# Performance work log

Hardware: AMD Instinct MI355X
Metric: run time of the kernel (lower is better)

The kernel has to match this reference:

```python
import jax, jax.numpy as jnp
import numpy as np
from jax.ops import segment_sum

N = 100000   # nodes
E = 6400000  # edges
D = 128      # input/output feature dim (d)
H = 15       # hidden width hard-coded in the module


def setup_inputs() -> dict:
    key = jax.random.key(0)
    ks = jax.random.split(key, 10)
    x = jax.random.normal(ks[0], (N, D), dtype=jnp.float32)
    edge_index = jax.random.randint(ks[1], (2, E), 0, N, dtype=jnp.int64)
    def glorot(k, shape):
        lim = np.sqrt(6.0 / (shape[0] + shape[1]))
        return jax.random.uniform(k, shape, jnp.float32, -lim, lim)
    W1 = glorot(ks[2], (D, H)); b1 = jnp.zeros((H,), jnp.float32)
    W2 = glorot(ks[3], (H, H)); b2 = jnp.zeros((H,), jnp.float32)
    W3 = glorot(ks[4], (H, H)); b3 = jnp.zeros((H,), jnp.float32)
    Wc = glorot(ks[5], (H, D)); bc = jnp.zeros((D,), jnp.float32)
    return {"x": x, "edge_index": edge_index,
            "W1": W1, "b1": b1, "W2": W2, "b2": b2,
            "W3": W3, "b3": b3, "Wc": Wc, "bc": bc}


def _gcn_norm(edge_index, n_nodes):
    # PyG GCNConv default: add self-loops, symmetric normalization.
    loops = jnp.arange(n_nodes, dtype=edge_index.dtype)
    row = jnp.concatenate([edge_index[0], loops])  # source
    col = jnp.concatenate([edge_index[1], loops])  # target (aggregation index)
    deg = segment_sum(jnp.ones_like(col, dtype=jnp.float32), col, num_segments=n_nodes)
    dinv = jnp.where(deg > 0, jax.lax.rsqrt(deg), 0.0)
    norm = dinv[row] * dinv[col]  # [E+N]
    return row, col, norm


def _gcn_conv(x, W, b, row, col, norm, n_nodes):
    h = x @ W                                   # [N, out]
    msg = h[row] * norm[:, None]                # gather + scale
    agg = segment_sum(msg, col, num_segments=n_nodes)
    return agg + b


def reference(x, edge_index, W1, b1, W2, b2, W3, b3, Wc, bc):
    row, col, norm = _gcn_norm(edge_index, N)
    h = jax.nn.relu(_gcn_conv(x, W1, b1, row, col, norm, N))
    h = jax.nn.relu(_gcn_conv(h, W2, b2, row, col, norm, N))
    h = jax.nn.relu(_gcn_conv(h, W3, b3, row, col, norm, N))
    return h @ Wc + bc
```

## Files before the change

### kernel.cpp

```cpp
#include <hip/hip_runtime.h>
#include <hip/hip_fp16.h>

#define DD 128
#define HH 15
#define BSHIFT 8
#define BUCK (1 << BSHIFT)
#define NBUCK 391
#define CAP 18432
#define CHUNK 4096
#define ABLK 512


__global__ __launch_bounds__(512) void init_gcur(int* __restrict__ gcur) {
    int i = threadIdx.x;
    if (i < NBUCK) gcur[i] = i * CAP;
}


__global__ __launch_bounds__(512) void partA(const int* __restrict__ row, const int* __restrict__ col,
                      int* __restrict__ gcur, unsigned* __restrict__ tmp, int E) {
    __shared__ int histo[NBUCK];
    __shared__ int hbase[NBUCK];
    __shared__ int hscan[NBUCK];
    __shared__ int wsum[8];
    __shared__ int s_total;
    __shared__ unsigned staged[CHUNK];
    __shared__ int saddr[CHUNK];
    int tid = threadIdx.x;
    int start = blockIdx.x * CHUNK;
    for (int i = tid; i < NBUCK; i += ABLK) histo[i] = 0;
    __syncthreads();
    unsigned pk[8]; unsigned short lp[8]; unsigned short bk[8];
    for (int k = 0; k < 8; ++k) {
        int e = start + k * ABLK + tid;
        bk[k] = 0xFFFF;
        if (e < E) {
            int cc = col[e];
            int b = cc >> BSHIFT;
            int rr = row[e];
            pk[k] = (unsigned)rr | ((unsigned)(cc & (BUCK - 1)) << 17);
            bk[k] = (unsigned short)b;
            lp[k] = (unsigned short)atomicAdd(&histo[b], 1);
        }
    }
    __syncthreads();
    int lane = tid & 63, wv = tid >> 6;
    int v = (tid < NBUCK) ? histo[tid] : 0;
    int s = v;
#pragma unroll
    for (int off = 1; off < 64; off <<= 1) {
        int u = __shfl_up(s, off, 64);
        if (lane >= off) s += u;
    }
    if (lane == 63) wsum[wv] = s;
    __syncthreads();
    if (tid == 0) {
        int r = 0;
        for (int i = 0; i < 8; ++i) { int u = wsum[i]; wsum[i] = r; r += u; }
        s_total = r;
    }
    __syncthreads();
    if (tid < NBUCK) {
        int excl = s + wsum[wv] - v;
        hscan[tid] = excl;
        if (v > 0) hbase[tid] = atomicAdd(&gcur[tid], v);
    }
    __syncthreads();
    for (int k = 0; k < 8; ++k) {
        if (bk[k] != 0xFFFF) {
            int b = bk[k];
            int slot = hscan[b] + lp[k];
            saddr[slot]  = min(hbase[b] + lp[k], NBUCK * CAP - 1);
            staged[slot] = pk[k];
        }
    }
    __syncthreads();
    int tot = s_total;
    for (int k = tid; k < tot; k += ABLK)
        tmp[saddr[k]] = staged[k];
}


__global__ __launch_bounds__(512) void scanC(const int* __restrict__ gcur,
                                             int* __restrict__ cbase,
                                             int* __restrict__ rowptr, int N) {
    __shared__ int wsum[8];
    int t = threadIdx.x, lane = t & 63, wv = t >> 6;
    int v = 0;
    if (t < NBUCK) v = min(gcur[t] - t * CAP, CAP);
    int s = v;
#pragma unroll
    for (int off = 1; off < 64; off <<= 1) {
        int u = __shfl_up(s, off, 64);
        if (lane >= off) s += u;
    }
    if (lane == 63) wsum[wv] = s;
    __syncthreads();
    int total = 0;
    if (t == 0) { int r = 0; for (int i = 0; i < 8; ++i) { int u = wsum[i]; wsum[i] = r; r += u; } total = r; }
    __syncthreads();
    if (t < NBUCK) cbase[t] = s + wsum[wv] - v;
    if (t == 0) { cbase[NBUCK] = total; rowptr[N] = total; }
}


__global__ __launch_bounds__(1024) void partB(const int* __restrict__ cbase, const unsigned* __restrict__ tmp,
                      int* __restrict__ rowptr, float* __restrict__ dinv,
                      int* __restrict__ csr_row, int N) {
    __shared__ int hist[BUCK];
    __shared__ int cur[BUCK];
    __shared__ int wsum[4];
    int b = blockIdx.x;
    int node0 = b << BSHIFT;
    int nn = min(BUCK, N - node0);
    int tid = threadIdx.x;
    if (tid < BUCK) hist[tid] = 0;
    __syncthreads();
    int base = cbase[b];
    int cnt  = cbase[b + 1] - base;
    const unsigned* te = tmp + (size_t)b * CAP;
    for (int e = tid; e < cnt; e += 1024)
        atomicAdd(&hist[te[e] >> 17], 1);
    __syncthreads();
    int lane = tid & 63, wv = tid >> 6;
    int d0 = (tid < BUCK) ? hist[tid] : 0;
    int s = d0;
#pragma unroll
    for (int off = 1; off < 64; off <<= 1) {
        int u = __shfl_up(s, off, 64);
        if (lane >= off) s += u;
    }
    if (tid < BUCK && lane == 63) wsum[wv] = s;
    __syncthreads();
    if (tid == 0) { int r = 0; for (int i = 0; i < 4; ++i) { int u = wsum[i]; wsum[i] = r; r += u; } }
    __syncthreads();
    if (tid < BUCK) {
        int excl = s + wsum[wv] - d0;
        cur[tid] = base + excl;
        if (tid < nn) {
            rowptr[node0 + tid] = base + excl;
            dinv[node0 + tid] = rsqrtf((float)(d0 + 1));
        }
    }
    __syncthreads();
    for (int e = tid; e < cnt; e += 1024) {
        unsigned v2 = te[e];
        int lc = (int)(v2 >> 17);
        int pos = atomicAdd(&cur[lc], 1);
        csr_row[pos] = (int)(v2 & 0x1FFFFu);
    }
}


__global__ void gemm1_kernel(const float* __restrict__ x, const float* __restrict__ W,
                             const float* __restrict__ dinv, __half* __restrict__ hs) {
    __shared__ float Wl[DD * HH];
    __shared__ float xs[16 * DD];
    int tid = threadIdx.x;
    for (int i = tid; i < DD * HH; i += 256) Wl[i] = W[i];
    size_t base = (size_t)blockIdx.x * 16 * DD;
    const float4* xv = (const float4*)(x + base);
    float4* xsv = (float4*)xs;
    xsv[tid]       = xv[tid];
    xsv[tid + 256] = xv[tid + 256];
    __syncthreads();
    int g = tid >> 4, f = tid & 15;
    int n = blockIdx.x * 16 + g;
    float val = 0.f;
    if (f < HH) {
        const float* xrow = xs + g * DD;
        float acc = 0.f;
#pragma unroll 8
        for (int k = 0; k < DD; ++k) acc += xrow[k] * Wl[k * HH + f];
        val = acc * dinv[n];
    }
    hs[(size_t)n * 16 + f] = __float2half(val);
}


__global__ void gemm_mid_kernel(const float* __restrict__ agg, const float* __restrict__ bias,
                                const float* __restrict__ W, const float* __restrict__ dinv,
                                __half* __restrict__ hs) {
    __shared__ float Wl[HH * HH];
    __shared__ float s_in[256];
    int tid = threadIdx.x;
    if (tid < HH * HH) Wl[tid] = W[tid];
    int n0 = blockIdx.x * 16;
    int g = tid >> 4, f = tid & 15;
    int n = n0 + g;
    if (f < HH) {
        float v = agg[(size_t)n * 16 + f] + bias[f];
        s_in[tid] = v > 0.f ? v : 0.f;
    }
    __syncthreads();
    float val = 0.f;
    if (f < HH) {
        const float* in = s_in + g * 16;
        float acc = 0.f;
#pragma unroll
        for (int k = 0; k < HH; ++k) acc += in[k] * Wl[k * HH + f];
        val = acc * dinv[n];
    }
    hs[(size_t)n * 16 + f] = __float2half(val);
}


struct alignas(16) H8 { __half2 h[4]; };

__device__ inline void acc8(float4& a0, float4& a1, const H8& v) {
    float2 f0 = __half22float2(v.h[0]);
    float2 f1 = __half22float2(v.h[1]);
    float2 f2 = __half22float2(v.h[2]);
    float2 f3 = __half22float2(v.h[3]);
    a0.x += f0.x; a0.y += f0.y; a0.z += f1.x; a0.w += f1.y;
    a1.x += f2.x; a1.y += f2.y; a1.z += f3.x; a1.w += f3.y;
}

__device__ inline float4 shfl_down4(float4 v, int off) {
    v.x = __shfl_down(v.x, off, 64);
    v.y = __shfl_down(v.y, off, 64);
    v.z = __shfl_down(v.z, off, 64);
    v.w = __shfl_down(v.w, off, 64);
    return v;
}

__global__ void aggregate_kernel(const int* __restrict__ rowptr, const int* __restrict__ csr_row,
                                 const float* __restrict__ dinv, const __half* __restrict__ hs,
                                 float* __restrict__ agg, int N) {
    int wid = (blockIdx.x * 256 + threadIdx.x) >> 6;
    int lane = threadIdx.x & 63;
    int sub = lane & 15;
    int c = wid * 4 + (lane >> 4);
    int q = sub & 1, eg = sub >> 1;
    int s = 0, epe = 0;
    if (c < N) { s = rowptr[c]; epe = rowptr[c + 1]; }
    const H8* h8 = (const H8*)hs;
    float4 a0 = make_float4(0.f, 0.f, 0.f, 0.f), a1 = a0;
    int e = s + eg;
    for (; e + 24 < epe; e += 32) {
        int i0 = csr_row[e];
        int i1 = csr_row[e + 8];
        int i2 = csr_row[e + 16];
        int i3 = csr_row[e + 24];
        H8 v0 = h8[((size_t)i0 << 1) + q];
        H8 v1 = h8[((size_t)i1 << 1) + q];
        H8 v2 = h8[((size_t)i2 << 1) + q];
        H8 v3 = h8[((size_t)i3 << 1) + q];
        acc8(a0, a1, v0); acc8(a0, a1, v1); acc8(a0, a1, v2); acc8(a0, a1, v3);
    }
    for (; e < epe; e += 8) {
        H8 v = h8[((size_t)csr_row[e] << 1) + q];
        acc8(a0, a1, v);
    }
#define RED4(off) { float4 t0_ = shfl_down4(a0, off); float4 t1_ = shfl_down4(a1, off); \
                    a0.x += t0_.x; a0.y += t0_.y; a0.z += t0_.z; a0.w += t0_.w; \
                    a1.x += t1_.x; a1.y += t1_.y; a1.z += t1_.z; a1.w += t1_.w; }
    RED4(8) RED4(4) RED4(2)
#undef RED4
    if (sub < 2 && c < N) {
        float d = dinv[c];
        H8 sv = h8[((size_t)c << 1) + q];
        float2 s0 = __half22float2(sv.h[0]);
        float2 s1 = __half22float2(sv.h[1]);
        float2 s2 = __half22float2(sv.h[2]);
        float2 s3 = __half22float2(sv.h[3]);
        float4 o0, o1;
        o0.x = d * (a0.x + s0.x); o0.y = d * (a0.y + s0.y);
        o0.z = d * (a0.z + s1.x); o0.w = d * (a0.w + s1.y);
        o1.x = d * (a1.x + s2.x); o1.y = d * (a1.y + s2.y);
        o1.z = d * (a1.z + s3.x); o1.w = d * (a1.w + s3.y);
        ((float4*)agg)[((size_t)c << 2) + q * 2]     = o0;
        ((float4*)agg)[((size_t)c << 2) + q * 2 + 1] = o1;
    }
}


__global__ void gemm_out_kernel(const float* __restrict__ agg, const float* __restrict__ bias,
                                const float* __restrict__ Wc, const float* __restrict__ bc,
                                float* __restrict__ out, int N) {
    __shared__ float Wl[HH * DD];
    __shared__ float s_in[256];
    int tid = threadIdx.x;
    for (int i = tid; i < HH * DD; i += 256) Wl[i] = Wc[i];
    int n0 = blockIdx.x * 16;
    {
        int gg = tid >> 4, ff = tid & 15;
        int n = n0 + gg;
        float v = 0.f;
        if (ff < HH && n < N) v = agg[(size_t)n * 16 + ff] + bias[ff];
        s_in[tid] = v > 0.f ? v : 0.f;
    }
    __syncthreads();
    int g = tid >> 7, f = tid & 127;
    float bcf = bc[f];
#pragma unroll
    for (int it = 0; it < 8; ++it) {
        int nl = it * 2 + g;
        int n = n0 + nl;
        const float* in = s_in + nl * 16;
        float acc = bcf;
#pragma unroll
        for (int k = 0; k < HH; ++k) acc += in[k] * Wl[k * DD + f];
        if (n < N) out[(size_t)n * DD + f] = acc;
    }
}


extern "C" void kernel_launch(void* const* d_in, const int* in_sizes, int n_in,
                              void* d_out, int out_size, void* d_ws, size_t ws_size,
                              hipStream_t stream) {
    const float* x  = (const float*)d_in[0];
    const int*   ei = (const int*)d_in[1];
    const float* W1 = (const float*)d_in[2];
    const float* b1 = (const float*)d_in[3];
    const float* W2 = (const float*)d_in[4];
    const float* b2 = (const float*)d_in[5];
    const float* W3 = (const float*)d_in[6];
    const float* b3 = (const float*)d_in[7];
    const float* Wc = (const float*)d_in[8];
    const float* bc = (const float*)d_in[9];
    float* out = (float*)d_out;

    int N = in_sizes[0] / DD;
    int E = in_sizes[1] / 2;
    const int* row = ei;
    const int* col = ei + E;

    char* ws = (char*)d_ws;
    size_t off = 0;
    auto alloc = [&](size_t bytes) {
        void* p = ws + off;
        off += (bytes + 255) & ~(size_t)255;
        return p;
    };
    float*    dinv    = (float*)   alloc((size_t)N * 4);
    int*      rowptr  = (int*)     alloc((size_t)(N + 1) * 4);
    int*      gcur    = (int*)     alloc((size_t)NBUCK * 4);
    int*      cbase   = (int*)     alloc((size_t)(NBUCK + 1) * 4);
    int*      csr_row = (int*)     alloc((size_t)E * 4 + 256);
    unsigned* tmp     = (unsigned*)alloc((size_t)NBUCK * CAP * 4);
    (void)n_in; (void)out_size; (void)ws_size;

    __half* hs  = (__half*)tmp;
    float*  agg = (float*)((char*)tmp + (size_t)N * 32);

    int eblocks = (E + CHUNK - 1) / CHUNK;

    init_gcur<<<1, 512, 0, stream>>>(gcur);
    partA<<<eblocks, ABLK, 0, stream>>>(row, col, gcur, tmp, E);
    scanC<<<1, 512, 0, stream>>>(gcur, cbase, rowptr, N);
    partB<<<NBUCK, 1024, 0, stream>>>(cbase, tmp, rowptr, dinv, csr_row, N);

    int nb16 = (N + 15) / 16;
    int aggblocks = (N + 15) / 16;

    gemm1_kernel<<<nb16, 256, 0, stream>>>(x, W1, dinv, hs);
    aggregate_kernel<<<aggblocks, 256, 0, stream>>>(rowptr, csr_row, dinv, hs, agg, N);
    gemm_mid_kernel<<<nb16, 256, 0, stream>>>(agg, b1, W2, dinv, hs);
    aggregate_kernel<<<aggblocks, 256, 0, stream>>>(rowptr, csr_row, dinv, hs, agg, N);
    gemm_mid_kernel<<<nb16, 256, 0, stream>>>(agg, b2, W3, dinv, hs);
    aggregate_kernel<<<aggblocks, 256, 0, stream>>>(rowptr, csr_row, dinv, hs, agg, N);
    gemm_out_kernel<<<nb16, 256, 0, stream>>>(agg, b3, Wc, bc, out, N);
}
```

Before: 398.9 us.

## Fuse bias, ReLU and hidden GEMM into aggregation kernel epilogue

Folds the mid-layer bias+ReLU+15x15 matmul into the aggregation kernel's epilogue, using wave shuffles to broadcast each node's 16 aggregated features. This removes two gemm_mid launches and the fp32 agg round trip between them. It also ping-pongs between two fp16 feature buffers and deepens the gather unroll from 4 to 8 loads in flight. The cost is more registers (launch bounds of 2 blocks per CU) and extra shuffles per node.

```diff
diff --git a/kernel.cpp b/kernel.cpp
--- a/kernel.cpp
+++ b/kernel.cpp
@@ -178,40 +178,11 @@
 }
 
 
-__global__ void gemm_mid_kernel(const float* __restrict__ agg, const float* __restrict__ bias,
-                                const float* __restrict__ W, const float* __restrict__ dinv,
-                                __half* __restrict__ hs) {
-    __shared__ float Wl[HH * HH];
-    __shared__ float s_in[256];
-    int tid = threadIdx.x;
-    if (tid < HH * HH) Wl[tid] = W[tid];
-    int n0 = blockIdx.x * 16;
-    int g = tid >> 4, f = tid & 15;
-    int n = n0 + g;
-    if (f < HH) {
-        float v = agg[(size_t)n * 16 + f] + bias[f];
-        s_in[tid] = v > 0.f ? v : 0.f;
-    }
-    __syncthreads();
-    float val = 0.f;
-    if (f < HH) {
-        const float* in = s_in + g * 16;
-        float acc = 0.f;
-#pragma unroll
-        for (int k = 0; k < HH; ++k) acc += in[k] * Wl[k * HH + f];
-        val = acc * dinv[n];
-    }
-    hs[(size_t)n * 16 + f] = __float2half(val);
-}
-
-
-struct alignas(16) H8 { __half2 h[4]; };
-
-__device__ inline void acc8(float4& a0, float4& a1, const H8& v) {
-    float2 f0 = __half22float2(v.h[0]);
-    float2 f1 = __half22float2(v.h[1]);
-    float2 f2 = __half22float2(v.h[2]);
-    float2 f3 = __half22float2(v.h[3]);
+__device__ inline void accU(float4& a0, float4& a1, const uint4& u) {
+    float2 f0 = __half22float2(*(const __half2*)&u.x);
+    float2 f1 = __half22float2(*(const __half2*)&u.y);
+    float2 f2 = __half22float2(*(const __half2*)&u.z);
+    float2 f3 = __half22float2(*(const __half2*)&u.w);
     a0.x += f0.x; a0.y += f0.y; a0.z += f1.x; a0.w += f1.y;
     a1.x += f2.x; a1.y += f2.y; a1.z += f3.x; a1.w += f3.y;
 }
@@ -224,54 +195,110 @@
     return v;
 }
 
-__global__ void aggregate_kernel(const int* __restrict__ rowptr, const int* __restrict__ csr_row,
-                                 const float* __restrict__ dinv, const __half* __restrict__ hs,
-                                 float* __restrict__ agg, int N) {
-    int wid = (blockIdx.x * 256 + threadIdx.x) >> 6;
-    int lane = threadIdx.x & 63;
+template <int FUSE>
+__global__ __launch_bounds__(256, 2)
+void aggregate_kernel(const int* __restrict__ rowptr, const int* __restrict__ csr_row,
+                      const float* __restrict__ dinv, const __half* __restrict__ hs,
+                      float* __restrict__ aggout,
+                      const float* __restrict__ bias, const float* __restrict__ W,
+                      __half* __restrict__ hsout, int N) {
+    __shared__ float Wl[16 * 16];
+    __shared__ float bs[16];
+    int tid = threadIdx.x;
+    if (FUSE) {
+        {
+            int k = tid >> 4, f = tid & 15;
+            Wl[tid] = (k < HH && f < HH) ? W[k * HH + f] : 0.f;
+        }
+        if (tid < 16) bs[tid] = (tid < HH) ? bias[tid] : 0.f;
+        __syncthreads();
+    }
+    int wid = (blockIdx.x * 256 + tid) >> 6;
+    int lane = tid & 63;
     int sub = lane & 15;
     int c = wid * 4 + (lane >> 4);
     int q = sub & 1, eg = sub >> 1;
     int s = 0, epe = 0;
     if (c < N) { s = rowptr[c]; epe = rowptr[c + 1]; }
-    const H8* h8 = (const H8*)hs;
+    const uint4* h8 = (const uint4*)hs;
     float4 a0 = make_float4(0.f, 0.f, 0.f, 0.f), a1 = a0;
     int e = s + eg;
-    for (; e + 24 < epe; e += 32) {
-        int i0 = csr_row[e];
-        int i1 = csr_row[e + 8];
-        int i2 = csr_row[e + 16];
-        int i3 = csr_row[e + 24];
-        H8 v0 = h8[((size_t)i0 << 1) + q];
-        H8 v1 = h8[((size_t)i1 << 1) + q];
-        H8 v2 = h8[((size_t)i2 << 1) + q];
-        H8 v3 = h8[((size_t)i3 << 1) + q];
-        acc8(a0, a1, v0); acc8(a0, a1, v1); acc8(a0, a1, v2); acc8(a0, a1, v3);
-    }
-    for (; e < epe; e += 8) {
-        H8 v = h8[((size_t)csr_row[e] << 1) + q];
-        acc8(a0, a1, v);
+    for (; e + 56 < epe; e += 64) {
+        int i0 = csr_row[e];      int i1 = csr_row[e + 8];
+        int i2 = csr_row[e + 16]; int i3 = csr_row[e + 24];
+        int i4 = csr_row[e + 32]; int i5 = csr_row[e + 40];
+        int i6 = csr_row[e + 48]; int i7 = csr_row[e + 56];
+        uint4 v0 = h8[((size_t)i0 << 1) + q];
+        uint4 v1 = h8[((size_t)i1 << 1) + q];
+        uint4 v2 = h8[((size_t)i2 << 1) + q];
+        uint4 v3 = h8[((size_t)i3 << 1) + q];
+        uint4 v4 = h8[((size_t)i4 << 1) + q];
+        uint4 v5 = h8[((size_t)i5 << 1) + q];
+        uint4 v6 = h8[((size_t)i6 << 1) + q];
+        uint4 v7 = h8[((size_t)i7 << 1) + q];
+        accU(a0, a1, v0); accU(a0, a1, v1); accU(a0, a1, v2); accU(a0, a1, v3);
+        accU(a0, a1, v4); accU(a0, a1, v5); accU(a0, a1, v6); accU(a0, a1, v7);
+    }
+    for (; e + 8 < epe; e += 16) {
+        int i0 = csr_row[e]; int i1 = csr_row[e + 8];
+        uint4 v0 = h8[((size_t)i0 << 1) + q];
+        uint4 v1 = h8[((size_t)i1 << 1) + q];
+        accU(a0, a1, v0); accU(a0, a1, v1);
+    }
+    if (e < epe) {
+        uint4 v0 = h8[((size_t)csr_row[e] << 1) + q];
+        accU(a0, a1, v0);
     }
 #define RED4(off) { float4 t0_ = shfl_down4(a0, off); float4 t1_ = shfl_down4(a1, off); \
                     a0.x += t0_.x; a0.y += t0_.y; a0.z += t0_.z; a0.w += t0_.w; \
                     a1.x += t1_.x; a1.y += t1_.y; a1.z += t1_.z; a1.w += t1_.w; }
     RED4(8) RED4(4) RED4(2)
 #undef RED4
+    float d = (c < N) ? dinv[c] : 0.f;
+    float4 o0 = make_float4(0.f, 0.f, 0.f, 0.f), o1 = o0;
     if (sub < 2 && c < N) {
-        float d = dinv[c];
-        H8 sv = h8[((size_t)c << 1) + q];
-        float2 s0 = __half22float2(sv.h[0]);
-        float2 s1 = __half22float2(sv.h[1]);
-        float2 s2 = __half22float2(sv.h[2]);
-        float2 s3 = __half22float2(sv.h[3]);
-        float4 o0, o1;
+        uint4 su = h8[((size_t)c << 1) + q];
+        float2 s0 = __half22float2(*(const __half2*)&su.x);
+        float2 s1 = __half22float2(*(const __half2*)&su.y);
+        float2 s2 = __half22float2(*(const __half2*)&su.z);
+        float2 s3 = __half22float2(*(const __half2*)&su.w);
         o0.x = d * (a0.x + s0.x); o0.y = d * (a0.y + s0.y);
         o0.z = d * (a0.z + s1.x); o0.w = d * (a0.w + s1.y);
         o1.x = d * (a1.x + s2.x); o1.y = d * (a1.y + s2.y);
         o1.z = d * (a1.z + s3.x); o1.w = d * (a1.w + s3.y);
-        ((float4*)agg)[((size_t)c << 2) + q * 2]     = o0;
-        ((float4*)agg)[((size_t)c << 2) + q * 2 + 1] = o1;
-    }
+    }
+    if (!FUSE) {
+        if (sub < 2 && c < N) {
+            ((float4*)aggout)[((size_t)c << 2) + q * 2]     = o0;
+            ((float4*)aggout)[((size_t)c << 2) + q * 2 + 1] = o1;
+        }
+        return;
+    }
+    if (sub < 2) {
+        int bb = q * 8;
+        o0.x += bs[bb + 0]; o0.y += bs[bb + 1]; o0.z += bs[bb + 2]; o0.w += bs[bb + 3];
+        o1.x += bs[bb + 4]; o1.y += bs[bb + 5]; o1.z += bs[bb + 6]; o1.w += bs[bb + 7];
+        o0.x = fmaxf(o0.x, 0.f); o0.y = fmaxf(o0.y, 0.f);
+        o0.z = fmaxf(o0.z, 0.f); o0.w = fmaxf(o0.w, 0.f);
+        o1.x = fmaxf(o1.x, 0.f); o1.y = fmaxf(o1.y, 0.f);
+        o1.z = fmaxf(o1.z, 0.f); o1.w = fmaxf(o1.w, 0.f);
+    }
+    int base = lane & ~15;
+    float va[8], vb[8];
+    va[0] = __shfl(o0.x, base, 64); va[1] = __shfl(o0.y, base, 64);
+    va[2] = __shfl(o0.z, base, 64); va[3] = __shfl(o0.w, base, 64);
+    va[4] = __shfl(o1.x, base, 64); va[5] = __shfl(o1.y, base, 64);
+    va[6] = __shfl(o1.z, base, 64); va[7] = __shfl(o1.w, base, 64);
+    vb[0] = __shfl(o0.x, base + 1, 64); vb[1] = __shfl(o0.y, base + 1, 64);
+    vb[2] = __shfl(o0.z, base + 1, 64); vb[3] = __shfl(o0.w, base + 1, 64);
+    vb[4] = __shfl(o1.x, base + 1, 64); vb[5] = __shfl(o1.y, base + 1, 64);
+    vb[6] = __shfl(o1.z, base + 1, 64); vb[7] = __shfl(o1.w, base + 1, 64);
+    float acc = 0.f;
+#pragma unroll
+    for (int k = 0; k < 8; ++k) acc += va[k] * Wl[k * 16 + sub];
+#pragma unroll
+    for (int k = 0; k < 8; ++k) acc += vb[k] * Wl[(8 + k) * 16 + sub];
+    if (c < N) hsout[(size_t)c * 16 + sub] = __float2half(acc * d);
 }
 
 
@@ -341,8 +368,9 @@
     unsigned* tmp     = (unsigned*)alloc((size_t)NBUCK * CAP * 4);
     (void)n_in; (void)out_size; (void)ws_size;
 
-    __half* hs  = (__half*)tmp;
-    float*  agg = (float*)((char*)tmp + (size_t)N * 32);
+    __half* hsA = (__half*)tmp;
+    __half* hsB = (__half*)((char*)tmp + (size_t)N * 32);
+    float*  agg = (float*)((char*)tmp + (size_t)N * 64);
 
     int eblocks = (E + CHUNK - 1) / CHUNK;
 
@@ -354,11 +382,12 @@
     int nb16 = (N + 15) / 16;
     int aggblocks = (N + 15) / 16;
 
-    gemm1_kernel<<<nb16, 256, 0, stream>>>(x, W1, dinv, hs);
-    aggregate_kernel<<<aggblocks, 256, 0, stream>>>(rowptr, csr_row, dinv, hs, agg, N);
-    gemm_mid_kernel<<<nb16, 256, 0, stream>>>(agg, b1, W2, dinv, hs);
-    aggregate_kernel<<<aggblocks, 256, 0, stream>>>(rowptr, csr_row, dinv, hs, agg, N);
-    gemm_mid_kernel<<<nb16, 256, 0, stream>>>(agg, b2, W3, dinv, hs);
-    aggregate_kernel<<<aggblocks, 256, 0, stream>>>(rowptr, csr_row, dinv, hs, agg, N);
+    gemm1_kernel<<<nb16, 256, 0, stream>>>(x, W1, dinv, hsA);
+    aggregate_kernel<1><<<aggblocks, 256, 0, stream>>>(rowptr, csr_row, dinv, hsA,
+                                                       nullptr, b1, W2, hsB, N);
+    aggregate_kernel<1><<<aggblocks, 256, 0, stream>>>(rowptr, csr_row, dinv, hsB,
+                                                       nullptr, b2, W3, hsA, N);
+    aggregate_kernel<0><<<aggblocks, 256, 0, stream>>>(rowptr, csr_row, dinv, hsA,
+                                                       agg, nullptr, nullptr, nullptr, N);
     gemm_out_kernel<<<nb16, 256, 0, stream>>>(agg, b3, Wc, bc, out, N);
 }
```

Result: no change. 396.3 us (-0.6%).
